# Optimization experiments

Hardware: AMD Instinct MI355X
Metric: run time of the kernel (lower is better)

The kernel has to match this reference:

```python
import jax, jax.numpy as jnp
import numpy as np

N_NODES = 100000
N_EDGES = 3200000
N_FEAT = 512
N_CLASS = 40
HIDDEN = 16


def _agnn(x, src, dst, beta, num_nodes):
    # PyG AGNNConv: cosine-similarity attention, softmax over incoming edges.
    norm = jnp.linalg.norm(x, axis=1, keepdims=True)
    x_norm = x / jnp.maximum(norm, 1e-12)
    # per-edge logits: beta * <x_norm_dst, x_norm_src>
    alpha = beta * jnp.sum(x_norm[dst] * x_norm[src], axis=1)  # [E]
    # segment softmax over destination nodes
    m = jax.ops.segment_max(alpha, dst, num_segments=num_nodes)  # [N]
    e = jnp.exp(alpha - m[dst])
    s = jax.ops.segment_sum(e, dst, num_segments=num_nodes)  # [N]
    w = e / jnp.maximum(s[dst], 1e-16)  # [E]
    # weighted aggregation of source features to destination
    return jax.ops.segment_sum(x[src] * w[:, None], dst, num_segments=num_nodes)


def setup_inputs() -> dict:
    key = jax.random.key(0)
    ks = jax.random.split(key, 7)
    x = jax.random.normal(ks[0], (N_NODES, N_FEAT), dtype=jnp.float32)
    edge_index = jax.random.randint(ks[1], (2, N_EDGES), 0, N_NODES, dtype=jnp.int32)
    lin1_w = jax.random.normal(ks[2], (HIDDEN, N_FEAT), dtype=jnp.float32) * (1.0 / np.sqrt(N_FEAT))
    lin1_b = jax.random.normal(ks[3], (HIDDEN,), dtype=jnp.float32) * 0.01
    beta2 = jnp.ones((1,), dtype=jnp.float32)
    lin2_w = jax.random.normal(ks[4], (N_CLASS, HIDDEN), dtype=jnp.float32) * (1.0 / np.sqrt(HIDDEN))
    lin2_b = jax.random.normal(ks[5], (N_CLASS,), dtype=jnp.float32) * 0.01
    return {"x": x, "edge_index": edge_index, "lin1_w": lin1_w, "lin1_b": lin1_b,
            "beta2": beta2, "lin2_w": lin2_w, "lin2_b": lin2_b}


def reference(x, edge_index, lin1_w, lin1_b, beta2, lin2_w, lin2_b):
    src, dst = edge_index[0], edge_index[1]
    n = x.shape[0]
    # eval mode: dropout is identity
    h = jax.nn.relu(x @ lin1_w.T + lin1_b)          # [N, 16]
    h = _agnn(h, src, dst, jnp.float32(1.0), n)     # prop1: beta fixed at 1
    h = _agnn(h, src, dst, beta2[0], n)             # prop2: learnable beta
    logits = h @ lin2_w.T + lin2_b                  # [N, C]
    return jax.nn.log_softmax(logits, axis=1)
```

## Files before the change

### kernel.cpp

```cpp
#include <hip/hip_runtime.h>

#define N_NODES 100000
#define N_EDGES 3200000
#define N_FEAT  512
#define HID     16
#define N_CLASS 40

#define BSHIFT  9
#define BMASK   ((1 << BSHIFT) - 1)
#define NB      196
#define CAP     18432
#define EPB     4096
#define EC_CAP  9216

#define BIN_BLOCKS  ((N_EDGES + EPB - 1) / EPB)
#define NT_TILES    (N_NODES / 16)
#define LIN1_BLOCKS ((NT_TILES + 3) / 4)

typedef __attribute__((ext_vector_type(8))) short bf16x8;
typedef __attribute__((ext_vector_type(4))) float f32x4;

__device__ inline short2 split_bf(float v) {
    const unsigned u = __float_as_uint(v);
    const short hi = (short)(u >> 16);
    const float hf = __uint_as_float(u & 0xFFFF0000u);
    const short lo = (short)(__float_as_uint(v - hf) >> 16);
    return make_short2(hi, lo);
}
__device__ inline unsigned short f2bf_rtn(float v) {
    unsigned u = __float_as_uint(v);
    u += 0x7FFFu + ((u >> 16) & 1u);
    return (unsigned short)(u >> 16);
}
__device__ inline float bf2f(unsigned short u) {
    return __uint_as_float(((unsigned)u) << 16);
}

struct BinSmem {
    int hist[NB]; int lofs[NB]; int base[NB]; int rk[NB];
    int buf[256]; int stage[EPB]; unsigned short sbkt[EPB];
};
struct Lin1Smem { short bfH[16 * 64 * 8]; short bfL[16 * 64 * 8]; };

__device__ void bin_body(char* smemraw,
                         const int* __restrict__ src,
                         const int* __restrict__ dst,
                         int* __restrict__ cursor,
                         int* __restrict__ binned) {
    BinSmem& sm = *(BinSmem*)smemraw;
    const int t = threadIdx.x;
    for (int i = t; i < NB; i += 256) { sm.hist[i] = 0; sm.rk[i] = 0; }
    __syncthreads();

    const int e0 = blockIdx.x * EPB;
    int bk[EPB / 256];
    int vv[EPB / 256];
#pragma unroll
    for (int k = 0; k < EPB / 256; k++) {
        const int e = e0 + k * 256 + t;
        if (e < N_EDGES) {
            const int d = dst[e], s = src[e];
            bk[k] = d >> BSHIFT;
            vv[k] = (s << BSHIFT) | (d & BMASK);
            atomicAdd(&sm.hist[bk[k]], 1);
        } else bk[k] = -1;
    }
    __syncthreads();

    {
        const int v = (t < NB) ? sm.hist[t] : 0;
        sm.buf[t] = v; __syncthreads();
        for (int o = 1; o < 256; o <<= 1) {
            const int a = (t >= o) ? sm.buf[t - o] : 0;
            __syncthreads();
            sm.buf[t] += a;
            __syncthreads();
        }
        if (t < NB) sm.lofs[t] = sm.buf[t] - v;
    }
    if (t < NB && sm.hist[t] > 0)
        sm.base[t] = t * CAP + atomicAdd(&cursor[t], sm.hist[t]);

#pragma unroll
    for (int k = 0; k < EPB / 256; k++) {
        if (bk[k] >= 0) {
            const int r = atomicAdd(&sm.rk[bk[k]], 1);
            const int slot = sm.lofs[bk[k]] + r;
            sm.stage[slot] = vv[k];
            sm.sbkt[slot] = (unsigned short)bk[k];
        }
    }
    __syncthreads();

    const int nloc = min(EPB, N_EDGES - e0);
    for (int s2 = t; s2 < nloc; s2 += 256) {
        const int b = sm.sbkt[s2];
        binned[sm.base[b] + (s2 - sm.lofs[b])] = sm.stage[s2];
    }
}

__device__ void lin1_body(char* smemraw, int lblk,
                          const float* __restrict__ x,
                          const float* __restrict__ w1,
                          const float* __restrict__ b1,
                          unsigned short* __restrict__ xnb,
                          float* __restrict__ normv) {
    Lin1Smem& sm = *(Lin1Smem*)smemraw;
    const int t = threadIdx.x;
    for (int f = t; f < 16 * 64; f += 256) {
        const int kt  = f >> 6;
        const int ln  = f & 63;
        const int col = ln & 15;
        const int k0  = kt * 32 + (ln >> 4) * 8;
        const float4 v0 = *(const float4*)(w1 + col * N_FEAT + k0);
        const float4 v1 = *(const float4*)(w1 + col * N_FEAT + k0 + 4);
        bf16x8 hh, ll;
        short2 r;
        r = split_bf(v0.x); hh[0] = r.x; ll[0] = r.y;
        r = split_bf(v0.y); hh[1] = r.x; ll[1] = r.y;
        r = split_bf(v0.z); hh[2] = r.x; ll[2] = r.y;
        r = split_bf(v0.w); hh[3] = r.x; ll[3] = r.y;
        r = split_bf(v1.x); hh[4] = r.x; ll[4] = r.y;
        r = split_bf(v1.y); hh[5] = r.x; ll[5] = r.y;
        r = split_bf(v1.z); hh[6] = r.x; ll[6] = r.y;
        r = split_bf(v1.w); hh[7] = r.x; ll[7] = r.y;
        ((bf16x8*)sm.bfH)[f] = hh;
        ((bf16x8*)sm.bfL)[f] = ll;
    }
    __syncthreads();

    const int wv   = t >> 6;
    const int l    = t & 63;
    const int tile = lblk * 4 + wv;
    if (tile >= NT_TILES) return;

    const int r0 = tile * 16;
    const float* xp = x + (size_t)(r0 + (l & 15)) * N_FEAT + ((l >> 4) * 8);

    f32x4 acc = {0.f, 0.f, 0.f, 0.f};
    float4 c0 = *(const float4*)(xp);
    float4 c1 = *(const float4*)(xp + 4);
#pragma unroll
    for (int kt = 0; kt < 16; ++kt) {
        float4 n0, n1;
        if (kt < 15) {
            n0 = *(const float4*)(xp + (kt + 1) * 32);
            n1 = *(const float4*)(xp + (kt + 1) * 32 + 4);
        }
        bf16x8 ah, al;
        short2 r;
        r = split_bf(c0.x); ah[0] = r.x; al[0] = r.y;
        r = split_bf(c0.y); ah[1] = r.x; al[1] = r.y;
        r = split_bf(c0.z); ah[2] = r.x; al[2] = r.y;
        r = split_bf(c0.w); ah[3] = r.x; al[3] = r.y;
        r = split_bf(c1.x); ah[4] = r.x; al[4] = r.y;
        r = split_bf(c1.y); ah[5] = r.x; al[5] = r.y;
        r = split_bf(c1.z); ah[6] = r.x; al[6] = r.y;
        r = split_bf(c1.w); ah[7] = r.x; al[7] = r.y;
        const bf16x8 bh = ((const bf16x8*)sm.bfH)[kt * 64 + l];
        const bf16x8 bl = ((const bf16x8*)sm.bfL)[kt * 64 + l];
        acc = __builtin_amdgcn_mfma_f32_16x16x32_bf16(ah, bh, acc, 0, 0, 0);
        acc = __builtin_amdgcn_mfma_f32_16x16x32_bf16(al, bh, acc, 0, 0, 0);
        acc = __builtin_amdgcn_mfma_f32_16x16x32_bf16(ah, bl, acc, 0, 0, 0);
        c0 = n0; c1 = n1;
    }

    const float bias = b1[l & 15];
#pragma unroll
    for (int r = 0; r < 4; ++r) {
        const float v = fmaxf(acc[r] + bias, 0.f);
        float ss = v * v;
        ss += __shfl_xor(ss, 1); ss += __shfl_xor(ss, 2);
        ss += __shfl_xor(ss, 4); ss += __shfl_xor(ss, 8);
        const float nrm = sqrtf(ss);
        const float rn  = 1.f / fmaxf(nrm, 1e-12f);
        const int row = r0 + (l >> 4) * 4 + r;
        xnb[(size_t)row * HID + (l & 15)] = f2bf_rtn(v * rn);
        if ((l & 15) == 0) normv[row] = nrm;
    }
}

__global__ __launch_bounds__(256) void k_bin_lin1(const int* __restrict__ src,
                                                  const int* __restrict__ dst,
                                                  int* __restrict__ cursor,
                                                  int* __restrict__ binned,
                                                  const float* __restrict__ x,
                                                  const float* __restrict__ w1,
                                                  const float* __restrict__ b1,
                                                  unsigned short* __restrict__ xnb,
                                                  float* __restrict__ normv) {
    __shared__ __align__(16) char smem[sizeof(Lin1Smem) > sizeof(BinSmem)
                                       ? sizeof(Lin1Smem) : sizeof(BinSmem)];
    if (blockIdx.x < BIN_BLOCKS)
        bin_body(smem, src, dst, cursor, binned);
    else
        lin1_body(smem, blockIdx.x - BIN_BLOCKS, x, w1, b1, xnb, normv);
}

__global__ __launch_bounds__(512) void k_csr(const int* __restrict__ cursor,
                                             int* __restrict__ binned,
                                             int* __restrict__ row_start,
                                             unsigned short* __restrict__ row_cnt) {
    __shared__ int cnts[512];
    __shared__ int cur[512];
    __shared__ int buf[512];
    __shared__ int lcsr[CAP];

    const int t = threadIdx.x;
    const int b = blockIdx.x;
    const int s0 = b * CAP;
    const int n = cursor[b];

    cnts[t] = 0;
    __syncthreads();
    for (int i = t; i < n; i += 512)
        atomicAdd(&cnts[binned[s0 + i] & BMASK], 1);
    __syncthreads();

    {
        const int v = cnts[t];
        buf[t] = v; __syncthreads();
        for (int o = 1; o < 512; o <<= 1) {
            const int a = (t >= o) ? buf[t - o] : 0;
            __syncthreads();
            buf[t] += a;
            __syncthreads();
        }
        cur[t] = buf[t] - v;
        const int node = (b << BSHIFT) + t;
        if (node < N_NODES) {
            row_start[node] = s0 + cur[t];
            row_cnt[node]   = (unsigned short)v;
        }
    }
    __syncthreads();

    for (int i = t; i < n; i += 512) {
        const int v = binned[s0 + i];
        const int p = atomicAdd(&cur[v & BMASK], 1);
        lcsr[p] = v >> BSHIFT;
    }
    __syncthreads();

    for (int i = t; i < n; i += 512) binned[s0 + i] = lcsr[i];
}

template <int LAST>
__global__ __launch_bounds__(256) void k_agnn(const int* __restrict__ row_start,
                                              const unsigned short* __restrict__ row_cnt,
                                              const int* __restrict__ csr_src,
                                              const unsigned short* __restrict__ xnb,
                                              const float* __restrict__ normv,
                                              const float* __restrict__ betap,
                                              const float* __restrict__ w2,
                                              const float* __restrict__ b2,
                                              float* __restrict__ out,
                                              unsigned short* __restrict__ outb,
                                              float* __restrict__ out_norm) {
    __shared__ int ldsCsr[EC_CAP];
    __shared__ float w2s[HID][N_CLASS + 1];
    __shared__ float b2s[N_CLASS];
    __shared__ int sRs0, sNE;

    const int t256 = threadIdx.x;
    const int node = blockIdx.x * 256 + t256;
    const bool alive = node < N_NODES;

    if (LAST) {
        for (int i = t256; i < N_CLASS * HID; i += 256)
            w2s[i % HID][i / HID] = w2[i];
        if (t256 < N_CLASS) b2s[t256] = b2[t256];
    }

    const int rs  = alive ? row_start[node] : 0;
    const int cnt = alive ? (int)row_cnt[node] : 0;

    if (t256 == 0) {
        const int base = blockIdx.x * 256;
        const int last = min(base + 256, N_NODES) - 1;
        const int r0 = row_start[base];
        sRs0 = r0;
        sNE  = row_start[last] + (int)row_cnt[last] - r0;
    }
    __syncthreads();
    const int rs0 = sRs0;
    const int nStage = min(sNE, EC_CAP);
    for (int i = t256; i < nStage; i += 256)
        ldsCsr[i] = csr_src[rs0 + i];
    __syncthreads();

    const float beta  = betap ? betap[0] : 1.0f;
    const float shift = fabsf(beta);
    const int off = rs - rs0;

    const int nodeSafe = alive ? node : 0;
    const bf16x8* xd = (const bf16x8*)(xnb + (size_t)nodeSafe * HID);
    const bf16x8 dlo = xd[0], dhi = xd[1];
    float dd[16];
#pragma unroll
    for (int i = 0; i < 8; i++) {
        dd[i]     = bf2f((unsigned short)dlo[i]);
        dd[i + 8] = bf2f((unsigned short)dhi[i]);
    }

    int mcnt = cnt;
#pragma unroll
    for (int m = 1; m < 64; m <<= 1) mcnt = max(mcnt, __shfl_xor(mcnt, m));

    float acc[16];
#pragma unroll
    for (int i = 0; i < 16; i++) acc[i] = 0.f;
    float swl = 0.f;

    bool ok = (0 < cnt);
    int sidx = 0;
    if (ok) { const int p = off; sidx = (p < nStage) ? ldsCsr[p] : csr_src[rs]; }
    const bf16x8* xs0 = (const bf16x8*)(xnb + (size_t)sidx * HID);
    bf16x8 slo = xs0[0], shi = xs0[1];
    float nj = normv[sidx];

    for (int t = 0; t < mcnt; ++t) {
        const bool ok2 = (t + 1 < cnt);
        int sidx2 = 0;
        if (ok2) {
            const int p = off + t + 1;
            sidx2 = (p < nStage) ? ldsCsr[p] : csr_src[rs + t + 1];
        }
        const bf16x8* xs2 = (const bf16x8*)(xnb + (size_t)sidx2 * HID);
        const bf16x8 slo2 = xs2[0], shi2 = xs2[1];
        const float nj2 = normv[sidx2];

        float sr[16];
#pragma unroll
        for (int i = 0; i < 8; i++) {
            sr[i]     = bf2f((unsigned short)slo[i]);
            sr[i + 8] = bf2f((unsigned short)shi[i]);
        }
        float p0 = 0.f, p1 = 0.f, p2 = 0.f, p3 = 0.f;
#pragma unroll
        for (int i = 0; i < 4; i++) {
            p0 += sr[i]      * dd[i];
            p1 += sr[i + 4]  * dd[i + 4];
            p2 += sr[i + 8]  * dd[i + 8];
            p3 += sr[i + 12] * dd[i + 12];
        }
        const float dot = (p0 + p1) + (p2 + p3);
        const float w = ok ? __expf(beta * dot - shift) : 0.f;
        swl += w;
        const float wn = w * nj;
#pragma unroll
        for (int i = 0; i < 16; i++) acc[i] += wn * sr[i];

        slo = slo2; shi = shi2; nj = nj2; ok = ok2;
    }

    const float inv = 1.f / fmaxf(swl, 1e-16f);
    float v[16];
#pragma unroll
    for (int i = 0; i < 16; i++) v[i] = acc[i] * inv;

    if (!LAST) {
        float ss = 0.f;
#pragma unroll
        for (int i = 0; i < 16; i++) ss += v[i] * v[i];
        const float nrm = sqrtf(ss);
        const float rn  = 1.f / fmaxf(nrm, 1e-12f);
        if (alive) {
            bf16x8 o0, o1;
#pragma unroll
            for (int i = 0; i < 8; i++) {
                o0[i] = (short)f2bf_rtn(v[i] * rn);
                o1[i] = (short)f2bf_rtn(v[i + 8] * rn);
            }
            bf16x8* orow = (bf16x8*)(outb + (size_t)node * HID);
            orow[0] = o0; orow[1] = o1;
            out_norm[node] = nrm;
        }
    } else {
        float lg[N_CLASS];
#pragma unroll
        for (int j = 0; j < N_CLASS; j++) lg[j] = b2s[j];
#pragma unroll
        for (int k = 0; k < HID; k++) {
            const float vk = v[k];
#pragma unroll
            for (int j = 0; j < N_CLASS; j++) lg[j] += vk * w2s[k][j];
        }
        float m = -3.0e38f;
#pragma unroll
        for (int j = 0; j < N_CLASS; j++) m = fmaxf(m, lg[j]);
        float s = 0.f;
#pragma unroll
        for (int j = 0; j < N_CLASS; j++) s += __expf(lg[j] - m);
        const float lse = m + __logf(s);
        if (alive) {
            float4* orow = (float4*)(out + (size_t)node * N_CLASS);
#pragma unroll
            for (int q = 0; q < N_CLASS / 4; q++) {
                float4 o;
                o.x = lg[q * 4 + 0] - lse;
                o.y = lg[q * 4 + 1] - lse;
                o.z = lg[q * 4 + 2] - lse;
                o.w = lg[q * 4 + 3] - lse;
                orow[q] = o;
            }
        }
    }
}

extern "C" void kernel_launch(void* const* d_in, const int* in_sizes, int n_in,
                              void* d_out, int out_size, void* d_ws, size_t ws_size,
                              hipStream_t stream) {
    const float* x     = (const float*)d_in[0];
    const int*   ei    = (const int*)  d_in[1];
    const float* w1    = (const float*)d_in[2];
    const float* b1    = (const float*)d_in[3];
    const float* beta2 = (const float*)d_in[4];
    const float* w2    = (const float*)d_in[5];
    const float* b2    = (const float*)d_in[6];
    float* out = (float*)d_out;

    const int* srcp = ei;
    const int* dstp = ei + N_EDGES;

    unsigned short* xnb1 = (unsigned short*)d_ws;
    unsigned short* xnb2 = xnb1 + (size_t)N_NODES * HID;
    float* norm1 = (float*)(xnb2 + (size_t)N_NODES * HID);
    float* norm2 = norm1 + N_NODES;
    int* row_start = (int*)(norm2 + N_NODES);
    unsigned short* row_cnt = (unsigned short*)(row_start + N_NODES);
    int* cursor = (int*)(row_cnt + N_NODES + (N_NODES & 1));
    int* binned = cursor + NB + 2;

    const int agnnGrid = (N_NODES + 255) / 256;

    hipMemsetAsync(cursor, 0, NB * sizeof(int), stream);

    k_bin_lin1<<<BIN_BLOCKS + LIN1_BLOCKS, 256, 0, stream>>>(
        srcp, dstp, cursor, binned, x, w1, b1, xnb1, norm1);

    k_csr<<<NB, 512, 0, stream>>>(cursor, binned, row_start, row_cnt);

    k_agnn<0><<<agnnGrid, 256, 0, stream>>>(row_start, row_cnt, binned, xnb1,
                                            norm1, nullptr, nullptr, nullptr,
                                            nullptr, xnb2, norm2);
    k_agnn<1><<<agnnGrid, 256, 0, stream>>>(row_start, row_cnt, binned, xnb2,
                                            norm2, beta2, w2, b2,
                                            out, nullptr, nullptr);
}
```

Measured before the change: 175.1 us.

## Split each node's edge loop across four lanes in AGNN kernels

The AGNN aggregation kernels now assign four threads per destination node instead of one. Each lane walks every fourth incoming edge, and the partial accumulators and weight sums are combined with xor shuffles. In the final layer the 40-class projection and log-softmax are also split across the four lanes. The aim is to shorten the per-warp serial loop, which is bounded by the maximum degree in the wave, and to expose more parallel gather loads. The cost is 4x more blocks, redundant per-node loads of the destination features, shuffle reductions, and a smaller LDS staging buffer for CSR indices.

```diff
diff --git a/kernel.cpp b/kernel.cpp
--- a/kernel.cpp
+++ b/kernel.cpp
@@ -11,7 +11,7 @@
 #define NB      196
 #define CAP     18432
 #define EPB     4096
-#define EC_CAP  9216
+#define EC_CAP  3072
 
 #define BIN_BLOCKS  ((N_EDGES + EPB - 1) / EPB)
 #define NT_TILES    (N_NODES / 16)
@@ -263,7 +263,8 @@
     __shared__ int sRs0, sNE;
 
     const int t256 = threadIdx.x;
-    const int node = blockIdx.x * 256 + t256;
+    const int ls   = t256 & 3;
+    const int node = blockIdx.x * 64 + (t256 >> 2);
     const bool alive = node < N_NODES;
 
     if (LAST) {
@@ -276,8 +277,8 @@
     const int cnt = alive ? (int)row_cnt[node] : 0;
 
     if (t256 == 0) {
-        const int base = blockIdx.x * 256;
-        const int last = min(base + 256, N_NODES) - 1;
+        const int base = blockIdx.x * 64;
+        const int last = min(base + 64, N_NODES) - 1;
         const int r0 = row_start[base];
         sRs0 = r0;
         sNE  = row_start[last] + (int)row_cnt[last] - r0;
@@ -303,7 +304,7 @@
         dd[i + 8] = bf2f((unsigned short)dhi[i]);
     }
 
-    int mcnt = cnt;
+    int mcnt = (cnt + 3) >> 2;
 #pragma unroll
     for (int m = 1; m < 64; m <<= 1) mcnt = max(mcnt, __shfl_xor(mcnt, m));
 
@@ -312,19 +313,20 @@
     for (int i = 0; i < 16; i++) acc[i] = 0.f;
     float swl = 0.f;
 
-    bool ok = (0 < cnt);
+    bool ok = (ls < cnt);
     int sidx = 0;
-    if (ok) { const int p = off; sidx = (p < nStage) ? ldsCsr[p] : csr_src[rs]; }
+    if (ok) { const int p = off + ls; sidx = (p < nStage) ? ldsCsr[p] : csr_src[rs + ls]; }
     const bf16x8* xs0 = (const bf16x8*)(xnb + (size_t)sidx * HID);
     bf16x8 slo = xs0[0], shi = xs0[1];
     float nj = normv[sidx];
 
     for (int t = 0; t < mcnt; ++t) {
-        const bool ok2 = (t + 1 < cnt);
+        const int e2 = 4 * (t + 1) + ls;
+        const bool ok2 = (e2 < cnt);
         int sidx2 = 0;
         if (ok2) {
-            const int p = off + t + 1;
-            sidx2 = (p < nStage) ? ldsCsr[p] : csr_src[rs + t + 1];
+            const int p = off + e2;
+            sidx2 = (p < nStage) ? ldsCsr[p] : csr_src[rs + e2];
         }
         const bf16x8* xs2 = (const bf16x8*)(xnb + (size_t)sidx2 * HID);
         const bf16x8 slo2 = xs2[0], shi2 = xs2[1];
@@ -354,6 +356,13 @@
         slo = slo2; shi = shi2; nj = nj2; ok = ok2;
     }
 
+#pragma unroll
+    for (int m = 1; m < 4; m <<= 1) {
+#pragma unroll
+        for (int i = 0; i < 16; i++) acc[i] += __shfl_xor(acc[i], m);
+        swl += __shfl_xor(swl, m);
+    }
+
     const float inv = 1.f / fmaxf(swl, 1e-16f);
     float v[16];
 #pragma unroll
@@ -365,7 +374,7 @@
         for (int i = 0; i < 16; i++) ss += v[i] * v[i];
         const float nrm = sqrtf(ss);
         const float rn  = 1.f / fmaxf(nrm, 1e-12f);
-        if (alive) {
+        if (alive && ls == 0) {
             bf16x8 o0, o1;
 #pragma unroll
             for (int i = 0; i < 8; i++) {
@@ -377,33 +386,29 @@
             out_norm[node] = nrm;
         }
     } else {
-        float lg[N_CLASS];
-#pragma unroll
-        for (int j = 0; j < N_CLASS; j++) lg[j] = b2s[j];
+        const int j0 = ls * 10;
+        float lg[10];
+#pragma unroll
+        for (int j = 0; j < 10; j++) lg[j] = b2s[j0 + j];
 #pragma unroll
         for (int k = 0; k < HID; k++) {
             const float vk = v[k];
 #pragma unroll
-            for (int j = 0; j < N_CLASS; j++) lg[j] += vk * w2s[k][j];
+            for (int j = 0; j < 10; j++) lg[j] += vk * w2s[k][j0 + j];
         }
         float m = -3.0e38f;
 #pragma unroll
-        for (int j = 0; j < N_CLASS; j++) m = fmaxf(m, lg[j]);
+        for (int j = 0; j < 10; j++) m = fmaxf(m, lg[j]);
+        m = fmaxf(m, __shfl_xor(m, 1)); m = fmaxf(m, __shfl_xor(m, 2));
         float s = 0.f;
 #pragma unroll
-        for (int j = 0; j < N_CLASS; j++) s += __expf(lg[j] - m);
+        for (int j = 0; j < 10; j++) s += __expf(lg[j] - m);
+        s += __shfl_xor(s, 1); s += __shfl_xor(s, 2);
         const float lse = m + __logf(s);
         if (alive) {
-            float4* orow = (float4*)(out + (size_t)node * N_CLASS);
-#pragma unroll
-            for (int q = 0; q < N_CLASS / 4; q++) {
-                float4 o;
-                o.x = lg[q * 4 + 0] - lse;
-                o.y = lg[q * 4 + 1] - lse;
-                o.z = lg[q * 4 + 2] - lse;
-                o.w = lg[q * 4 + 3] - lse;
-                orow[q] = o;
-            }
+            float* orow = out + (size_t)node * N_CLASS + j0;
+#pragma unroll
+            for (int j = 0; j < 10; j++) orow[j] = lg[j] - lse;
         }
     }
 }
@@ -432,7 +437,7 @@
     int* cursor = (int*)(row_cnt + N_NODES + (N_NODES & 1));
     int* binned = cursor + NB + 2;
 
-    const int agnnGrid = (N_NODES + 255) / 256;
+    const int agnnGrid = (N_NODES + 63) / 64;
 
     hipMemsetAsync(cursor, 0, NB * sizeof(int), stream);
 
```

Result: faster. 166.7 us, median of 2 (-4.8%).
